# Kernel tuning notes

Measured on AMD Instinct MI355X. Metric: run time of the kernel, lower is better.

Reference implementation:

```python
import jax, jax.numpy as jnp
import numpy as np

ATT = 16          # attention_size -> window = 2*ATT+1 = 33
HID = 512         # middle hidden size


def setup_inputs() -> dict:
    key = jax.random.key(0)
    ks = jax.random.split(key, 7)
    B, S, D_IN = 4, 2048, 256
    def xav(k, shape):
        fan_in, fan_out = shape[0], shape[1]
        std = np.sqrt(2.0 / (fan_in + fan_out))
        return jax.random.normal(k, shape, dtype=jnp.float32) * std
    return {
        "x": jax.random.normal(ks[0], (B, S, D_IN), dtype=jnp.float32),
        "Wq": xav(ks[1], (HID, HID)),
        "Wk": xav(ks[2], (HID, HID)),
        "Wv": xav(ks[3], (HID, HID)),
        "W0": xav(ks[4], (D_IN, HID)),
        "b0": jnp.zeros((1, 1, HID), dtype=jnp.float32),
        "W1": xav(ks[5], (HID, HID)),
        "b1": jnp.zeros((1, 1, HID), dtype=jnp.float32),
        "Wout": xav(ks[6], (HID, 2)),
        "bout": jnp.zeros((1, 1, 2), dtype=jnp.float32),
    }


def _local_windows(h, A):
    # h: [B, S, H] -> nei: [B, S, 2A+1, H], nei[b,t,j] = h[b, t+A-j] (zero padded)
    S = h.shape[1]
    padded = jnp.pad(h, ((0, 0), (A, A), (0, 0)))
    t = jnp.arange(S)[:, None]
    j = jnp.arange(2 * A + 1)[None, :]
    idx = t + 2 * A - j  # padded index of h[t + A - j]
    return padded[:, idx, :]


def reference(x, Wq, Wk, Wv, W0, b0, W1, b1, Wout, bout):
    scale = jnp.float32(np.sqrt(float(HID)))
    # pre-attention MLP layer(s)
    h = jax.nn.relu(x @ W0 + b0)                       # [B,S,H]
    nei = _local_windows(h, ATT)                       # [B,S,W,H]
    q = h @ Wq                                         # [B,S,H]
    k = nei @ Wk                                       # [B,S,W,H]
    v = nei @ Wv                                       # [B,S,W,H]
    dist = jnp.einsum('bsd,bswd->bsw', q, k) / scale   # [B,S,W]
    attn = jax.nn.softmax(dist, axis=-1)               # [B,S,W]
    ctx = jnp.einsum('bsw,bswd->bsd', attn, v)         # [B,S,H]
    # post-attention MLP layers
    h2 = jax.nn.relu(ctx @ W1 + b1)
    out = h2 @ Wout + bout                             # [B,S,2]
    return out, attn[:, :, None, :]  # attn shape [B,S,1,W] as in torch
```

## Files before the change

kernel.cpp:

```cpp
#include <hip/hip_runtime.h>

#define S_LEN 2048
#define HID 512
#define DIN 256
#define WIN 33
#define MROWS 8192
#define VTB 2080
#define VTROW 8320
#define SCALE_INV 0.04419417382415922f

typedef __attribute__((ext_vector_type(8))) short short8;
typedef __attribute__((ext_vector_type(4))) float f32x4;

__device__ __forceinline__ unsigned short f2bf(float f) {
    unsigned u = __builtin_bit_cast(unsigned, f);
    u += 0x7fffu + ((u >> 16) & 1u);
    return (unsigned short)(u >> 16);
}
__device__ __forceinline__ float bf2f(unsigned short h) {
    unsigned u = ((unsigned)h) << 16;
    return __builtin_bit_cast(float, u);
}
__device__ __forceinline__ void gl_lds16(const unsigned short* g, unsigned short* l) {
    __builtin_amdgcn_global_load_lds(
        (__attribute__((address_space(1))) unsigned int*)(g),
        (__attribute__((address_space(3))) unsigned int*)(l),
        16, 0, 0);
}

__global__ __launch_bounds__(256) void prep_kernel(
    const float* __restrict__ x,
    const float* __restrict__ Wq, const float* __restrict__ Wk,
    const float* __restrict__ Wv, const float* __restrict__ W0,
    const float* __restrict__ W1, const float* __restrict__ bout,
    unsigned short* __restrict__ xb, unsigned short* __restrict__ Wt0,
    unsigned short* __restrict__ Wtqkv, unsigned short* __restrict__ Wt1,
    unsigned short* __restrict__ Vt, float* __restrict__ outp)
{
    __shared__ float tile[32][33];
    const int blk = blockIdx.x, tid = threadIdx.x;
    if (blk < 2048) {
        int i = (blk * 256 + tid) * 4;
        float4 v = *(const float4*)(x + i);
        unsigned lo = (unsigned)f2bf(v.x) | ((unsigned)f2bf(v.y) << 16);
        unsigned hi = (unsigned)f2bf(v.z) | ((unsigned)f2bf(v.w) << 16);
        uint2 p; p.x = lo; p.y = hi;
        *(uint2*)(xb + i) = p;
    } else if (blk < 2064) {
        int i = ((blk - 2048) * 256 + tid) * 4;
        float4 o; o.x = bout[0]; o.y = bout[1]; o.z = bout[0]; o.w = bout[1];
        *(float4*)(outp + i) = o;
    } else if (blk < 2320) {
        int t = (blk - 2064) * 256 + tid;
        int v = t >> 7, s = t & 127;
        int b = s >> 5, p = s & 31;
        int off = (p < 16) ? p : (2048 + p);
        Vt[(size_t)v * VTROW + b * VTB + off] = 0;
    } else {
        int tt = blk - 2320;
        const float* in; unsigned short* out; int K, kt, nt;
        if (tt < 128) { in = W0; out = Wt0; K = DIN; kt = tt & 7; nt = tt >> 3; }
        else {
            int z = (tt - 128) >> 8, r = (tt - 128) & 255;
            kt = r & 15; nt = r >> 4; K = HID;
            if (z == 0)      { in = Wq; out = Wtqkv; }
            else if (z == 1) { in = Wk; out = Wtqkv + 512 * 512; }
            else if (z == 2) { in = Wv; out = Wtqkv + 2 * 512 * 512; }
            else             { in = W1; out = Wt1; }
        }
        int k0 = kt * 32, n0 = nt * 32;
        int tx = tid & 31, ty = tid >> 5;
        for (int j = 0; j < 32; j += 8)
            tile[ty + j][tx] = in[(size_t)(k0 + ty + j) * HID + n0 + tx];
        __syncthreads();
        for (int j = 0; j < 32; j += 8)
            out[(size_t)(n0 + ty + j) * K + k0 + tx] = f2bf(tile[tx][ty + j]);
    }
}

template<int K, int MODE>
__global__ __launch_bounds__(256) void gemm128_kernel(
    const unsigned short* __restrict__ A,
    const unsigned short* __restrict__ Bt,
    const float* __restrict__ bias,
    unsigned short* __restrict__ C0,
    unsigned short* __restrict__ C1,
    unsigned short* __restrict__ C2,
    const float* __restrict__ Wout,
    float* __restrict__ outp)
{
    __shared__ __align__(16) unsigned short SMEM[24576];
    const int tid = threadIdx.x;
    const int lane = tid & 63, wid = tid >> 6;
    const int bn = blockIdx.x, bm = blockIdx.y;
    const int wr = wid >> 1, wc = wid & 1;
    const int r16 = lane & 15, kq = lane >> 4;
    const int NT = K / 32;

    f32x4 acc[4][4] = {};

    const int c0 = tid, c1 = tid + 256;
    const unsigned short* aS0 = A + (size_t)(bm * 128 + (c0 & 127)) * K + (c0 >> 7) * 8;
    const unsigned short* aS1 = A + (size_t)(bm * 128 + (c1 & 127)) * K + (c1 >> 7) * 8;
    const unsigned short* bS0 = Bt + (size_t)(bn * 128 + (c0 & 127)) * K + (c0 >> 7) * 8;
    const unsigned short* bS1 = Bt + (size_t)(bn * 128 + (c1 & 127)) * K + (c1 >> 7) * 8;

    #define STAGE(buf, kt) do { \
        gl_lds16(aS0 + (kt) * 32, SMEM + (buf) * 8192 + c0 * 8); \
        gl_lds16(aS1 + (kt) * 32, SMEM + (buf) * 8192 + c1 * 8); \
        gl_lds16(bS0 + (kt) * 32, SMEM + (buf) * 8192 + 4096 + c0 * 8); \
        gl_lds16(bS1 + (kt) * 32, SMEM + (buf) * 8192 + 4096 + c1 * 8); \
    } while (0)

    STAGE(0, 0);
    STAGE(1, 1);
    int cur = 0;
    for (int kt = 0; kt < NT; ++kt) {
        if (kt + 2 < NT) {
            STAGE((cur + 2) % 3, kt + 2);
            asm volatile("s_waitcnt vmcnt(8)" ::: "memory");
        } else if (kt + 1 < NT) {
            asm volatile("s_waitcnt vmcnt(4)" ::: "memory");
        } else {
            asm volatile("s_waitcnt vmcnt(0)" ::: "memory");
        }
        __builtin_amdgcn_sched_barrier(0);
        __builtin_amdgcn_s_barrier();
        __builtin_amdgcn_sched_barrier(0);

        const unsigned short* ab = SMEM + cur * 8192;
        const unsigned short* bb = ab + 4096;
        short8 af[4], bfr[4];
        #pragma unroll
        for (int mi = 0; mi < 4; ++mi)
            af[mi] = *(const short8*)(ab + kq * 1024 + (wr * 64 + mi * 16 + r16) * 8);
        #pragma unroll
        for (int ni = 0; ni < 4; ++ni)
            bfr[ni] = *(const short8*)(bb + kq * 1024 + (wc * 64 + ni * 16 + r16) * 8);
        #pragma unroll
        for (int mi = 0; mi < 4; ++mi)
            #pragma unroll
            for (int ni = 0; ni < 4; ++ni)
                acc[mi][ni] = __builtin_amdgcn_mfma_f32_16x16x32_bf16(af[mi], bfr[ni], acc[mi][ni], 0, 0, 0);

        asm volatile("s_waitcnt lgkmcnt(0)" ::: "memory");
        __builtin_amdgcn_sched_barrier(0);
        __builtin_amdgcn_s_barrier();
        __builtin_amdgcn_sched_barrier(0);
        cur = (cur + 1) % 3;
    }
    #undef STAGE

    if constexpr (MODE == 0) {
        #pragma unroll
        for (int mi = 0; mi < 4; ++mi) {
            int row0 = bm * 128 + wr * 64 + mi * 16 + kq * 4;
            #pragma unroll
            for (int ni = 0; ni < 4; ++ni) {
                int col = bn * 128 + wc * 64 + ni * 16 + r16;
                float bv = bias[col];
                #pragma unroll
                for (int r = 0; r < 4; ++r) {
                    float v = fmaxf(acc[mi][ni][r] + bv, 0.0f);
                    C0[(size_t)(row0 + r) * HID + col] = f2bf(v);
                }
            }
        }
    } else if constexpr (MODE == 1) {
        if (bn < 8) {
            unsigned short* dst = (bn < 4) ? C0 : C1;
            int cb = (bn & 3) * 128 + wc * 64;
            #pragma unroll
            for (int mi = 0; mi < 4; ++mi) {
                int row0 = bm * 128 + wr * 64 + mi * 16 + kq * 4;
                #pragma unroll
                for (int ni = 0; ni < 4; ++ni) {
                    int col = cb + ni * 16 + r16;
                    #pragma unroll
                    for (int r = 0; r < 4; ++r)
                        dst[(size_t)(row0 + r) * HID + col] = f2bf(acc[mi][ni][r]);
                }
            }
        } else {
            const int bb  = (bm * 128) >> 11;
            const int tl0 = (bm * 128) & 2047;
            #pragma unroll
            for (int p = 0; p < 2; ++p) {
                if (wc == p) {
                    #pragma unroll
                    for (int mi = 0; mi < 4; ++mi) {
                        int ttw = wr * 64 + mi * 16 + kq * 4;
                        #pragma unroll
                        for (int ni = 0; ni < 4; ++ni) {
                            int vv = ni * 16 + r16;
                            unsigned lo = (unsigned)f2bf(acc[mi][ni][0]) | ((unsigned)f2bf(acc[mi][ni][1]) << 16);
                            unsigned hi = (unsigned)f2bf(acc[mi][ni][2]) | ((unsigned)f2bf(acc[mi][ni][3]) << 16);
                            uint2 pk; pk.x = lo; pk.y = hi;
                            *(uint2*)&SMEM[vv * 128 + (ttw ^ ((vv & 7) << 3))] = pk;
                        }
                    }
                }
                __syncthreads();
                #pragma unroll
                for (int it = 0; it < 4; ++it) {
                    int vv  = (tid >> 4) + it * 16;
                    int tt8 = (tid & 15) * 8;
                    uint4 q = *(const uint4*)&SMEM[vv * 128 + (tt8 ^ ((vv & 7) << 3))];
                    int vg = (bn - 8) * 128 + p * 64 + vv;
                    *(uint4*)(C2 + (size_t)vg * VTROW + bb * VTB + 16 + tl0 + tt8) = q;
                }
                __syncthreads();
            }
        }
    } else {
        float o0[16], o1[16];
        #pragma unroll
        for (int t2 = 0; t2 < 16; ++t2) { o0[t2] = 0.0f; o1[t2] = 0.0f; }
        #pragma unroll
        for (int ni = 0; ni < 4; ++ni) {
            int col = bn * 128 + wc * 64 + ni * 16 + r16;
            float bv = bias[col];
            float2 wv = *(const float2*)(Wout + col * 2);
            #pragma unroll
            for (int mi = 0; mi < 4; ++mi)
                #pragma unroll
                for (int r = 0; r < 4; ++r) {
                    float v = fmaxf(acc[mi][ni][r] + bv, 0.0f);
                    o0[mi * 4 + r] += v * wv.x;
                    o1[mi * 4 + r] += v * wv.y;
                }
        }
        #pragma unroll
        for (int s = 1; s < 16; s <<= 1)
            #pragma unroll
            for (int t2 = 0; t2 < 16; ++t2) {
                o0[t2] += __shfl_xor(o0[t2], s);
                o1[t2] += __shfl_xor(o1[t2], s);
            }
        if (r16 == 0) {
            #pragma unroll
            for (int mi = 0; mi < 4; ++mi)
                #pragma unroll
                for (int r = 0; r < 4; ++r) {
                    int row = bm * 128 + wr * 64 + mi * 16 + kq * 4 + r;
                    atomicAdd(&outp[(size_t)row * 2],     o0[mi * 4 + r]);
                    atomicAdd(&outp[(size_t)row * 2 + 1], o1[mi * 4 + r]);
                }
        }
    }
}

__global__ __launch_bounds__(256) void attn_kernel(
    const unsigned short* __restrict__ Qb,
    const unsigned short* __restrict__ Kb,
    const unsigned short* __restrict__ Vt,
    float* __restrict__ attn_out,
    unsigned short* __restrict__ ctx)
{
    __shared__ __align__(16) float Sl[4][32][66];
    __shared__ __align__(16) unsigned short Pl[32 * 64];
    const int tid = threadIdx.x;
    const int lane = tid & 63;
    const int w = tid >> 6;
    const int t0g = blockIdx.x * 32;
    const int b = t0g >> 11;
    const int t0 = t0g & 2047;
    const int r16 = lane & 15, kq = lane >> 4;

    f32x4 s[2][4] = {};
    const unsigned short* qbase = Qb + (size_t)t0g * HID + w * 128 + kq * 8;
    const unsigned short* kbase = Kb + (long)(t0g - 16) * HID + w * 128 + kq * 8;
    #pragma unroll
    for (int ks = 0; ks < 4; ++ks) {
        short8 a0 = *(const short8*)(qbase + (size_t)r16 * HID + ks * 32);
        short8 a1 = *(const short8*)(qbase + (size_t)(16 + r16) * HID + ks * 32);
        #pragma unroll
        for (int ni = 0; ni < 4; ++ni) {
            short8 bf = *(const short8*)(kbase + (size_t)(ni * 16 + r16) * HID + ks * 32);
            s[0][ni] = __builtin_amdgcn_mfma_f32_16x16x32_bf16(a0, bf, s[0][ni], 0, 0, 0);
            s[1][ni] = __builtin_amdgcn_mfma_f32_16x16x32_bf16(a1, bf, s[1][ni], 0, 0, 0);
        }
    }
    #pragma unroll
    for (int mi = 0; mi < 2; ++mi)
        #pragma unroll
        for (int ni = 0; ni < 4; ++ni)
            #pragma unroll
            for (int r = 0; r < 4; ++r)
                Sl[w][mi * 16 + kq * 4 + r][ni * 16 + r16] = s[mi][ni][r];
    __syncthreads();

    {
        const int i = tid >> 3;
        const int c8 = (tid & 7) * 8;
        float sv[8];
        #pragma unroll
        for (int cc = 0; cc < 8; ++cc) {
            float a = Sl[0][i][c8 + cc] + Sl[1][i][c8 + cc]
                    + Sl[2][i][c8 + cc] + Sl[3][i][c8 + cc];
            int m = c8 + cc;
            bool inb = (m >= i) && (m <= i + 32);
            int krow = t0 + m - 16;
            bool inseq = (krow >= 0) && (krow < S_LEN);
            sv[cc] = inb ? (inseq ? a * SCALE_INV : 0.0f) : -INFINITY;
        }
        float mx = sv[0];
        #pragma unroll
        for (int cc = 1; cc < 8; ++cc) mx = fmaxf(mx, sv[cc]);
        mx = fmaxf(mx, __shfl_xor(mx, 1));
        mx = fmaxf(mx, __shfl_xor(mx, 2));
        mx = fmaxf(mx, __shfl_xor(mx, 4));
        float es = 0.0f;
        #pragma unroll
        for (int cc = 0; cc < 8; ++cc) { sv[cc] = __expf(sv[cc] - mx); es += sv[cc]; }
        es += __shfl_xor(es, 1);
        es += __shfl_xor(es, 2);
        es += __shfl_xor(es, 4);
        float inv = 1.0f / es;
        unsigned short pb[8];
        #pragma unroll
        for (int cc = 0; cc < 8; ++cc) {
            float p = sv[cc] * inv;
            pb[cc] = f2bf(p);
            int m = c8 + cc;
            if (m >= i && m <= i + 32)
                attn_out[(size_t)(t0g + i) * WIN + (i + 32 - m)] = p;
        }
        uint4 pk;
        pk.x = (unsigned)pb[0] | ((unsigned)pb[1] << 16);
        pk.y = (unsigned)pb[2] | ((unsigned)pb[3] << 16);
        pk.z = (unsigned)pb[4] | ((unsigned)pb[5] << 16);
        pk.w = (unsigned)pb[6] | ((unsigned)pb[7] << 16);
        *(uint4*)((char*)Pl + i * 128 + ((c8 * 2) ^ ((i & 7) << 4))) = pk;
    }
    __syncthreads();

    f32x4 c[2][8] = {};
    const char* plb = (const char*)Pl;
    const unsigned short* vtb = Vt + (size_t)b * VTB + t0;
    #pragma unroll
    for (int ks = 0; ks < 2; ++ks) {
        int cb = ks * 64 + kq * 16;
        short8 a0 = *(const short8*)(plb + r16 * 128 + (cb ^ ((r16 & 7) << 4)));
        short8 a1 = *(const short8*)(plb + (16 + r16) * 128 + (cb ^ ((r16 & 7) << 4)));
        #pragma unroll
        for (int nd = 0; nd < 8; ++nd) {
            const unsigned short* vp = vtb + (size_t)(w * 128 + nd * 16 + r16) * VTROW + ks * 32 + kq * 8;
            short8 bf = *(const short8*)vp;
            c[0][nd] = __builtin_amdgcn_mfma_f32_16x16x32_bf16(a0, bf, c[0][nd], 0, 0, 0);
            c[1][nd] = __builtin_amdgcn_mfma_f32_16x16x32_bf16(a1, bf, c[1][nd], 0, 0, 0);
        }
    }
    #pragma unroll
    for (int mi = 0; mi < 2; ++mi) {
        int row0 = t0g + mi * 16 + kq * 4;
        #pragma unroll
        for (int nd = 0; nd < 8; ++nd) {
            int col = w * 128 + nd * 16 + r16;
            #pragma unroll
            for (int r = 0; r < 4; ++r)
                ctx[(size_t)(row0 + r) * HID + col] = f2bf(c[mi][nd][r]);
        }
    }
}

extern "C" void kernel_launch(void* const* d_in, const int* in_sizes, int n_in,
                              void* d_out, int out_size, void* d_ws, size_t ws_size,
                              hipStream_t stream)
{
    const float* x    = (const float*)d_in[0];
    const float* Wq   = (const float*)d_in[1];
    const float* Wk   = (const float*)d_in[2];
    const float* Wv   = (const float*)d_in[3];
    const float* W0   = (const float*)d_in[4];
    const float* b0   = (const float*)d_in[5];
    const float* W1   = (const float*)d_in[6];
    const float* b1   = (const float*)d_in[7];
    const float* Wout = (const float*)d_in[8];
    const float* bout = (const float*)d_in[9];

    char* ws = (char*)d_ws;
    unsigned short* xb    = (unsigned short*)(ws + 0);
    unsigned short* Wt0   = (unsigned short*)(ws + (4u  << 20));
    unsigned short* Wtqkv = (unsigned short*)(ws + 4456448u);
    unsigned short* Wt1   = (unsigned short*)(ws + 6029312u);
    unsigned short* hB    = (unsigned short*)(ws + (8u  << 20));
    unsigned short* Qb    = (unsigned short*)(ws + (16u << 20));
    unsigned short* Kb    = (unsigned short*)(ws + (24u << 20));
    unsigned short* Vt    = (unsigned short*)(ws + (32u << 20));
    unsigned short* ctxB  = (unsigned short*)(ws + (41u << 20));

    float* outp  = (float*)d_out;
    float* attnp = (float*)d_out + MROWS * 2;

    prep_kernel<<<3472, 256, 0, stream>>>(x, Wq, Wk, Wv, W0, W1, bout,
                                          xb, Wt0, Wtqkv, Wt1, Vt, outp);

    gemm128_kernel<DIN, 0><<<dim3(4, 64), 256, 0, stream>>>(
        xb, Wt0, b0, hB, nullptr, nullptr, nullptr, nullptr);

    gemm128_kernel<HID, 1><<<dim3(12, 64), 256, 0, stream>>>(
        hB, Wtqkv, nullptr, Qb, Kb, Vt, nullptr, nullptr);

    attn_kernel<<<256, 256, 0, stream>>>(Qb, Kb, Vt, attnp, ctxB);

    gemm128_kernel<HID, 2><<<dim3(4, 64), 256, 0, stream>>>(
        ctxB, Wt1, b1, nullptr, nullptr, nullptr, Wout, outp);
}
```

Before: 145.9 us.

## Move weight transposes and buffer init from prep into first GEMM grid

The prep kernel now only converts x and transposes W0. The Wq/Wk/Wv/W1 transposes, the Vt padding zeroing and the output bias init move into extra blocks of the first GEMM launch (grid widened from 4 to 25 columns). This shortens the serial prep stage and lets that independent work run alongside the first GEMM's compute blocks. The cost is a larger, imbalanced grid and a branch at the start of every GEMM block.

```diff
diff --git a/kernel.cpp b/kernel.cpp
--- a/kernel.cpp
+++ b/kernel.cpp
@@ -29,13 +29,8 @@
 }
 
 __global__ __launch_bounds__(256) void prep_kernel(
-    const float* __restrict__ x,
-    const float* __restrict__ Wq, const float* __restrict__ Wk,
-    const float* __restrict__ Wv, const float* __restrict__ W0,
-    const float* __restrict__ W1, const float* __restrict__ bout,
-    unsigned short* __restrict__ xb, unsigned short* __restrict__ Wt0,
-    unsigned short* __restrict__ Wtqkv, unsigned short* __restrict__ Wt1,
-    unsigned short* __restrict__ Vt, float* __restrict__ outp)
+    const float* __restrict__ x, const float* __restrict__ W0,
+    unsigned short* __restrict__ xb, unsigned short* __restrict__ Wt0)
 {
     __shared__ float tile[32][33];
     const int blk = blockIdx.x, tid = threadIdx.x;
@@ -46,35 +41,16 @@
         unsigned hi = (unsigned)f2bf(v.z) | ((unsigned)f2bf(v.w) << 16);
         uint2 p; p.x = lo; p.y = hi;
         *(uint2*)(xb + i) = p;
-    } else if (blk < 2064) {
-        int i = ((blk - 2048) * 256 + tid) * 4;
-        float4 o; o.x = bout[0]; o.y = bout[1]; o.z = bout[0]; o.w = bout[1];
-        *(float4*)(outp + i) = o;
-    } else if (blk < 2320) {
-        int t = (blk - 2064) * 256 + tid;
-        int v = t >> 7, s = t & 127;
-        int b = s >> 5, p = s & 31;
-        int off = (p < 16) ? p : (2048 + p);
-        Vt[(size_t)v * VTROW + b * VTB + off] = 0;
     } else {
-        int tt = blk - 2320;
-        const float* in; unsigned short* out; int K, kt, nt;
-        if (tt < 128) { in = W0; out = Wt0; K = DIN; kt = tt & 7; nt = tt >> 3; }
-        else {
-            int z = (tt - 128) >> 8, r = (tt - 128) & 255;
-            kt = r & 15; nt = r >> 4; K = HID;
-            if (z == 0)      { in = Wq; out = Wtqkv; }
-            else if (z == 1) { in = Wk; out = Wtqkv + 512 * 512; }
-            else if (z == 2) { in = Wv; out = Wtqkv + 2 * 512 * 512; }
-            else             { in = W1; out = Wt1; }
-        }
+        int tt = blk - 2048;
+        int kt = tt & 7, nt = tt >> 3;
         int k0 = kt * 32, n0 = nt * 32;
         int tx = tid & 31, ty = tid >> 5;
         for (int j = 0; j < 32; j += 8)
-            tile[ty + j][tx] = in[(size_t)(k0 + ty + j) * HID + n0 + tx];
+            tile[ty + j][tx] = W0[(size_t)(k0 + ty + j) * HID + n0 + tx];
         __syncthreads();
         for (int j = 0; j < 32; j += 8)
-            out[(size_t)(n0 + ty + j) * K + k0 + tx] = f2bf(tile[tx][ty + j]);
+            Wt0[(size_t)(n0 + ty + j) * DIN + k0 + tx] = f2bf(tile[tx][ty + j]);
     }
 }
 
@@ -87,7 +63,16 @@
     unsigned short* __restrict__ C1,
     unsigned short* __restrict__ C2,
     const float* __restrict__ Wout,
-    float* __restrict__ outp)
+    float* __restrict__ outp,
+    const float* __restrict__ Wqf,
+    const float* __restrict__ Wkf,
+    const float* __restrict__ Wvf,
+    const float* __restrict__ W1f,
+    const float* __restrict__ boutf,
+    unsigned short* __restrict__ WtqkvO,
+    unsigned short* __restrict__ Wt1O,
+    unsigned short* __restrict__ VtO,
+    float* __restrict__ outpO)
 {
     __shared__ __align__(16) unsigned short SMEM[24576];
     const int tid = threadIdx.x;
@@ -96,6 +81,42 @@
     const int wr = wid >> 1, wc = wid & 1;
     const int r16 = lane & 15, kq = lane >> 4;
     const int NT = K / 32;
+
+    if constexpr (MODE == 0) {
+        if (bn >= 4) {
+            if (bn < 20) {
+                float (*tile)[33] = (float(*)[33])SMEM;
+                int tt = (bn - 4) * 64 + bm;
+                int z = tt >> 8, r = tt & 255, kt = r & 15, nt = r >> 4;
+                const float* in; unsigned short* out;
+                if (z == 0)      { in = Wqf; out = WtqkvO; }
+                else if (z == 1) { in = Wkf; out = WtqkvO + 512 * 512; }
+                else if (z == 2) { in = Wvf; out = WtqkvO + 2 * 512 * 512; }
+                else             { in = W1f; out = Wt1O; }
+                int k0 = kt * 32, n0 = nt * 32;
+                int tx = tid & 31, ty = tid >> 5;
+                for (int j = 0; j < 32; j += 8)
+                    tile[ty + j][tx] = in[(size_t)(k0 + ty + j) * HID + n0 + tx];
+                __syncthreads();
+                for (int j = 0; j < 32; j += 8)
+                    out[(size_t)(n0 + ty + j) * HID + k0 + tx] = f2bf(tile[tx][ty + j]);
+            } else {
+                int idx = (bn - 20) * 64 + bm;
+                if (idx < 256) {
+                    int t = idx * 256 + tid;
+                    int v = t >> 7, s = t & 127;
+                    int b2 = s >> 5, p = s & 31;
+                    int off = (p < 16) ? p : (2048 + p);
+                    VtO[(size_t)v * VTROW + b2 * VTB + off] = 0;
+                } else if (idx < 272) {
+                    int i = ((idx - 256) * 256 + tid) * 4;
+                    float4 o; o.x = boutf[0]; o.y = boutf[1]; o.z = boutf[0]; o.w = boutf[1];
+                    *(float4*)(outpO + i) = o;
+                }
+            }
+            return;
+        }
+    }
 
     f32x4 acc[4][4] = {};
 
@@ -393,17 +414,19 @@
     float* outp  = (float*)d_out;
     float* attnp = (float*)d_out + MROWS * 2;
 
-    prep_kernel<<<3472, 256, 0, stream>>>(x, Wq, Wk, Wv, W0, W1, bout,
-                                          xb, Wt0, Wtqkv, Wt1, Vt, outp);
-
-    gemm128_kernel<DIN, 0><<<dim3(4, 64), 256, 0, stream>>>(
-        xb, Wt0, b0, hB, nullptr, nullptr, nullptr, nullptr);
+    prep_kernel<<<2176, 256, 0, stream>>>(x, W0, xb, Wt0);
+
+    gemm128_kernel<DIN, 0><<<dim3(25, 64), 256, 0, stream>>>(
+        xb, Wt0, b0, hB, nullptr, nullptr, nullptr, nullptr,
+        Wq, Wk, Wv, W1, bout, Wtqkv, Wt1, Vt, outp);
 
     gemm128_kernel<HID, 1><<<dim3(12, 64), 256, 0, stream>>>(
-        hB, Wtqkv, nullptr, Qb, Kb, Vt, nullptr, nullptr);
+        hB, Wtqkv, nullptr, Qb, Kb, Vt, nullptr, nullptr,
+        nullptr, nullptr, nullptr, nullptr, nullptr, nullptr, nullptr, nullptr, nullptr);
 
     attn_kernel<<<256, 256, 0, stream>>>(Qb, Kb, Vt, attnp, ctxB);
 
     gemm128_kernel<HID, 2><<<dim3(4, 64), 256, 0, stream>>>(
-        ctxB, Wt1, b1, nullptr, nullptr, nullptr, Wout, outp);
-}
+        ctxB, Wt1, b1, nullptr, nullptr, nullptr, Wout, outp,
+        nullptr, nullptr, nullptr, nullptr, nullptr, nullptr, nullptr, nullptr, nullptr);
+}
```

Result: slower. 153.3 us (+5.1%).
